# Performance work log

Measured on AMD Instinct MI355X. Metric: run time of the kernel, lower is better.

Reference implementation:

```python
import jax, jax.numpy as jnp
import numpy as np

W_REG = 3.0
N_CAND = 4
IOU_LEN = 15.0
BIG_COST = 1e8


def focal_cost(cls_pred, gt_labels, alpha=0.25, gamma=2.0, eps=1e-12):
    # cls_pred: [B,P,C] logits, gt_labels: [B,T] int -> [B,P,T]
    p = jax.nn.sigmoid(cls_pred)
    neg = -jnp.log(1.0 - p + eps) * (1.0 - alpha) * p ** gamma
    pos = -jnp.log(p + eps) * alpha * (1.0 - p) ** gamma
    B, P, _ = cls_pred.shape
    T = gt_labels.shape[1]
    idx = jnp.broadcast_to(gt_labels[:, None, :], (B, P, T))
    return jnp.take_along_axis(pos, idx, axis=2) - jnp.take_along_axis(neg, idx, axis=2)


def line_iou(pred, target, img_w, length=IOU_LEN):
    # pred: [B,P,O], target: [B,T,O] -> [B,P,T] (unaligned)
    px1, px2 = pred - length, pred + length
    tx1, tx2 = target - length, target + length
    ovr = jnp.minimum(px2[:, :, None, :], tx2[:, None, :, :]) - jnp.maximum(px1[:, :, None, :], tx1[:, None, :, :])
    union = jnp.maximum(px2[:, :, None, :], tx2[:, None, :, :]) - jnp.minimum(px1[:, :, None, :], tx1[:, None, :, :])
    invalid = ((target < 0) | (target >= img_w))[:, None, :, :]
    ovr = jnp.where(invalid, 0.0, ovr)
    union = jnp.where(invalid, 0.0, union)
    return ovr.sum(-1) / (union.sum(-1) + 1e-9)


def clrnet_assign(preds, targets, masks, img_w, img_h):
    B, P, _ = preds.shape
    T = targets.shape[1]
    w = float(img_w - 1)
    h = float(img_h - 1)
    pa = preds.at[..., 3].multiply(w).at[..., 6:].multiply(w)
    ta = targets.at[..., 3].multiply(w).at[..., 6:].multiply(w)
    p_off, t_off = pa[..., 6:], ta[..., 6:]

    # --- distance score (masked mean L1 over valid target x-offsets) ---
    tvalid = (t_off >= 0) & (t_off < img_w)                      # [B,T,O]
    cmask = tvalid[:, None, :, :]                                 # [B,1,T,O]
    clen = jnp.maximum(cmask.sum(-1).astype(pa.dtype), 1.0)      # [B,1,T]
    diff = jnp.abs(p_off[:, :, None, :] - t_off[:, None, :, :]) * cmask  # [B,P,T,O]
    distances = diff.sum(-1) / clen                               # [B,P,T]
    dist_max = jnp.maximum(distances.max(axis=(1, 2), keepdims=True), 1e-8)
    dist_score = 1.0 - distances / dist_max + 0.01

    # --- start-point score (euclidean on (y*(h), x)) ---
    ps = pa[..., 2:4].at[..., 0].multiply(h)
    ts = ta[..., 2:4].at[..., 0].multiply(h)
    start_d = jnp.sqrt(((ps[:, :, None, :] - ts[:, None, :, :]) ** 2).sum(-1))
    start_max = jnp.maximum(start_d.max(axis=(1, 2), keepdims=True), 1e-8)
    start_score = 1.0 - start_d / start_max + 0.01

    # --- theta score ---
    th_d = jnp.abs(pa[..., 4][:, :, None] - ta[..., 4][:, None, :]) * 180.0
    th_max = jnp.maximum(th_d.max(axis=(1, 2), keepdims=True), 1e-8)
    th_score = 1.0 - th_d / th_max + 0.01

    # --- total cost ---
    gt_labels = ta[..., 1].astype(jnp.int32)
    cls_cost = focal_cost(pa[..., :2], gt_labels)
    reg = (jnp.maximum(dist_score, 1e-3) * jnp.maximum(start_score, 1e-3)
           * jnp.maximum(th_score, 1e-3))
    total_cost = -(reg ** 2) * W_REG + cls_cost                   # [B,P,T]
    valid_t = (masks > 0)[:, None, :]                             # [B,1,T]
    total_cost = jnp.where(valid_t, total_cost, BIG_COST)

    # --- dynamic-k from line IoU ---
    liou = jnp.nan_to_num(line_iou(p_off, t_off, img_w), nan=0.0)
    liou = jnp.where(valid_t, liou, 0.0)
    k = min(N_CAND, P)
    topk_ious, _ = jax.lax.top_k(jnp.swapaxes(liou, 1, 2), k)     # [B,T,k]
    dynamic_ks = jnp.maximum(topk_ious.sum(-1).astype(jnp.int32), 1)
    dynamic_ks = jnp.where(masks > 0, dynamic_ks, 0)              # [B,T]

    # --- top-k lowest-cost priors per target, scatter into matching matrix ---
    _, topk_idx = jax.lax.top_k(-jnp.swapaxes(total_cost, 1, 2), k)  # [B,T,k]
    sel = (jnp.arange(k)[None, None, :] < dynamic_ks[:, :, None]).astype(total_cost.dtype)  # [B,T,k]
    one_hot_p = jax.nn.one_hot(topk_idx, P, dtype=total_cost.dtype)  # [B,T,k,P]
    matching = jnp.swapaxes((one_hot_p * sel[..., None]).sum(2), 1, 2)  # [B,P,T]

    # --- conflict resolution: a prior matched to >1 targets keeps argmin-cost one ---
    conflict = matching.sum(-1) > 1                               # [B,P]
    masked_cost = jnp.where(matching == 0, jnp.inf, total_cost)
    best_t = jnp.argmin(masked_cost, axis=2)                      # [B,P]
    new_m = jax.nn.one_hot(best_t, T, dtype=matching.dtype)
    matching = jnp.where(conflict[..., None], new_m, matching)

    has_match = matching.sum(-1) > 0.5
    t_idx = jnp.argmax(matching, axis=2)
    matched = jnp.where(has_match, t_idx, -1).astype(jnp.int32)
    return matched >= 0, matched


def setup_inputs() -> dict:
    key = jax.random.key(0)
    k1, k2, k3 = jax.random.split(key, 3)
    B, P, T, O = 32, 1000, 16, 72
    D = 6 + O
    preds = jax.random.uniform(k1, (B, P, D), dtype=jnp.float32)
    # slightly outside [0,1] so the invalid-offset masking path is exercised
    targets = jax.random.uniform(k2, (B, T, D), dtype=jnp.float32, minval=-0.05, maxval=1.05)
    masks = jax.random.randint(k3, (B, T), 0, 2).astype(jnp.int32)
    return {"preds": preds, "targets": targets, "masks": masks, "img_w": 800, "img_h": 320}


def reference(preds, targets, masks, img_w, img_h):
    return clrnet_assign(preds, targets, masks, img_w, img_h)
```

## Files before the change

### kernel.cpp

```cpp
#include <hip/hip_runtime.h>
#include <math.h>

#define B_ 32
#define P_ 1000
#define T_ 16
#define D_ 78
#define O_ 72
#define NXB 16
#define BIGC 100000000.0f

__global__ __launch_bounds__(1024, 8) void k1(
        const float* __restrict__ preds, const float* __restrict__ targets,
        const int* __restrict__ imgw_p, const int* __restrict__ imgh_p,
        float* __restrict__ dist, float* __restrict__ liou,
        float4* __restrict__ scal4, float* __restrict__ pths,
        float* __restrict__ pmax) {
    __shared__ float pred_s[64 * 81];
    __shared__ float2 tomg[T_ * O_];
    __shared__ float Spart[T_][4][64];
    __shared__ float wmax[16][3];
    __shared__ float cnt_s[T_], clen_s[T_], ts0_s[T_], ts1_s[T_], tth_s[T_];

    const int b = blockIdx.y, bx = blockIdx.x;
    const int p0 = bx * 64;
    const int rows = min(64, P_ - p0);
    const int tid = threadIdx.x;
    const float w = (float)(imgw_p[0] - 1);
    const float h = (float)(imgh_p[0] - 1);
    const float imgwf = (float)imgw_p[0];

    {
        const float4* gbase = (const float4*)(preds + ((size_t)b * P_ + p0) * D_);
        const int n4 = rows * D_ / 4;
        for (int i = tid; i < n4; i += 1024) {
            float4 v = gbase[i];
            int base = i * 4;
            int r = base / D_, c = base - r * D_;
#pragma unroll
            for (int k = 0; k < 4; ++k) {
                int cc = c + k, rr = r;
                if (cc >= D_) { cc -= D_; ++rr; }
                float x = (&v.x)[k];
                if (cc >= 6 || cc == 3) x *= w;
                pred_s[rr * 81 + cc] = x;
            }
        }
    }
    for (int i = tid; i < T_ * O_; i += 1024) {
        int t = i / O_, o = i - t * O_;
        float to = targets[((size_t)b * T_ + t) * D_ + 6 + o] * w;
        float m = (to >= 0.f && to < imgwf) ? 1.f : 0.f;
        tomg[((t >> 2) * O_ + o) * 4 + (t & 3)] = make_float2(to, m);
    }
    __syncthreads();
    if (tid < T_) {
        int t = tid;
        float c = 0.f;
        for (int o = 0; o < O_; ++o) c += tomg[((t >> 2) * O_ + o) * 4 + (t & 3)].y;
        cnt_s[t] = c;
        clen_s[t] = fmaxf(c, 1.f);
        const float* tr = targets + ((size_t)b * T_ + t) * D_;
        ts0_s[t] = tr[2] * h;
        ts1_s[t] = tr[3] * w;
        tth_s[t] = tr[4];
    }
    __syncthreads();

    {
        const int lane = tid & 63;
        const int wv = tid >> 6;
        const int tg = wv & 3;
        const int oq = wv >> 2;
        const float* lrow = pred_s + lane * 81;
        const float4* tg4 = (const float4*)(tomg + (size_t)tg * O_ * 4);
        const int o_lo = oq * 18;
        float S0 = 0.f, S1 = 0.f, S2 = 0.f, S3 = 0.f;
#pragma unroll
        for (int i = 0; i < 18; ++i) {
            int o = o_lo + i;
            float po = lrow[6 + o];
            float4 r0 = tg4[2 * o];
            float4 r1 = tg4[2 * o + 1];
            S0 += r0.y * fabsf(po - r0.x);
            S1 += r0.w * fabsf(po - r0.z);
            S2 += r1.y * fabsf(po - r1.x);
            S3 += r1.w * fabsf(po - r1.z);
        }
        Spart[4 * tg + 0][oq][lane] = S0;
        Spart[4 * tg + 1][oq][lane] = S1;
        Spart[4 * tg + 2][oq][lane] = S2;
        Spart[4 * tg + 3][oq][lane] = S3;
    }
    __syncthreads();

    const int th = tid >> 6, pl = tid & 63;
    const int p = p0 + pl;
    float ldm = 0.f, lsm = 0.f, ltm = 0.f;
    if (pl < rows) {
        float S = ((Spart[th][0][pl] + Spart[th][1][pl]) + Spart[th][2][pl]) + Spart[th][3][pl];
        float dv = S / clen_s[th];
        dist[(size_t)(b * T_ + th) * P_ + p] = dv;
        ldm = dv;
        float c30 = 30.f * cnt_s[th];
        liou[(size_t)(b * T_ + th) * P_ + p] = (c30 - S) / (c30 + S + 1e-9f);
        const float* prow = pred_s + pl * 81;
        float ps0 = prow[2] * h, ps1 = prow[3], pth = prow[4];
        float d0 = ps0 - ts0_s[th], d1 = ps1 - ts1_s[th];
        lsm = sqrtf(d0 * d0 + d1 * d1);
        ltm = fabsf(pth - tth_s[th]) * 180.f;
        if (th == 0) {
            float fc[2];
#pragma unroll
            for (int c = 0; c < 2; ++c) {
                float x = prow[c];
                float pc = 1.f / (1.f + expf(-x));
                float neg = -logf(1.f - pc + 1e-12f) * 0.75f * pc * pc;
                float pos = -logf(pc + 1e-12f) * 0.25f * (1.f - pc) * (1.f - pc);
                fc[c] = pos - neg;
            }
            scal4[(size_t)b * P_ + p] = make_float4(fc[0], fc[1], ps0, ps1);
            pths[(size_t)b * P_ + p] = pth;
        }
    }

    for (int off = 32; off; off >>= 1) {
        ldm = fmaxf(ldm, __shfl_xor(ldm, off, 64));
        lsm = fmaxf(lsm, __shfl_xor(lsm, off, 64));
        ltm = fmaxf(ltm, __shfl_xor(ltm, off, 64));
    }
    if (pl == 0) { wmax[th][0] = ldm; wmax[th][1] = lsm; wmax[th][2] = ltm; }
    __syncthreads();
    if (tid == 0) {
        float m0 = 0.f, m1 = 0.f, m2 = 0.f;
#pragma unroll
        for (int i = 0; i < 16; ++i) {
            m0 = fmaxf(m0, wmax[i][0]);
            m1 = fmaxf(m1, wmax[i][1]);
            m2 = fmaxf(m2, wmax[i][2]);
        }
        float* q = pmax + (size_t)(b * NXB + bx) * 3;
        q[0] = m0; q[1] = m1; q[2] = m2;
    }
}

__global__ __launch_bounds__(256) void k2(
        const float* __restrict__ targets, const int* __restrict__ masks,
        const int* __restrict__ imgw_p, const int* __restrict__ imgh_p,
        const float* __restrict__ dist, const float* __restrict__ liou,
        const float4* __restrict__ scal4, const float* __restrict__ pths,
        const float* __restrict__ pmax,
        int4* __restrict__ sel, float4* __restrict__ selc) {
    __shared__ float costL[1024];
    __shared__ float liouL[1024];

    const int wid = blockIdx.x;
    const int b = wid >> 4, t = wid & 15;
    const int tid = threadIdx.x;

    float dm = 0.f, sm = 0.f, tm = 0.f;
    for (int i = 0; i < NXB; ++i) {
        const float* q = pmax + (size_t)(b * NXB + i) * 3;
        dm = fmaxf(dm, q[0]); sm = fmaxf(sm, q[1]); tm = fmaxf(tm, q[2]);
    }
    dm = fmaxf(dm, 1e-8f); sm = fmaxf(sm, 1e-8f); tm = fmaxf(tm, 1e-8f);

    const float w = (float)(imgw_p[0] - 1);
    const float h = (float)(imgh_p[0] - 1);
    const float* tr = targets + (size_t)(b * T_ + t) * D_;
    const float ts0 = tr[2] * h, ts1 = tr[3] * w, tth = tr[4];
    int lab = (int)tr[1]; lab = lab < 0 ? 0 : (lab > 1 ? 1 : lab);
    const int mk = masks[b * T_ + t];

    const float* drow = dist + (size_t)(b * T_ + t) * P_;
    const float* lrow = liou + (size_t)(b * T_ + t) * P_;
    const float4* s4b = scal4 + (size_t)b * P_;
    const float* ptb = pths + (size_t)b * P_;

#pragma unroll
    for (int i = 0; i < 4; ++i) {
        int p = tid + 256 * i;
        if (p < P_) {
            float d = drow[p];
            float4 s4 = s4b[p];
            float pth = ptb[p];
            float dsc = 1.f - d / dm + 0.01f;
            float d0 = s4.z - ts0, d1 = s4.w - ts1;
            float ssc = 1.f - sqrtf(d0 * d0 + d1 * d1) / sm + 0.01f;
            float tsc = 1.f - fabsf(pth - tth) * 180.f / tm + 0.01f;
            float reg = fmaxf(dsc, 1e-3f) * fmaxf(ssc, 1e-3f) * fmaxf(tsc, 1e-3f);
            float c = -(reg * reg) * 3.f + (lab ? s4.y : s4.x);
            if (mk <= 0) c = BIGC;
            costL[p] = c;
            liouL[p] = lrow[p];
        } else {
            costL[p] = INFINITY;
            liouL[p] = -INFINITY;
        }
    }
    __syncthreads();
    if (tid >= 64) return;

    const int lane = tid;

    float sum = 0.f;
    for (int r = 0; r < 4; ++r) {
        float bv = -INFINITY; int bi = 0x7fffffff;
#pragma unroll
        for (int i = 0; i < 16; ++i) {
            int ix = lane + 64 * i;
            float v = liouL[ix];
            if (v > bv || (v == bv && ix < bi)) { bv = v; bi = ix; }
        }
        for (int off = 32; off; off >>= 1) {
            float ov = __shfl_xor(bv, off, 64);
            int oi = __shfl_xor(bi, off, 64);
            if (ov > bv || (ov == bv && oi < bi)) { bv = ov; bi = oi; }
        }
        sum += bv;
        if ((bi & 63) == lane) liouL[bi] = -INFINITY;
    }
    int dk = 0;
    if (mk > 0) {
        dk = (int)sum;
        if (dk < 1) dk = 1;
        if (dk > 4) dk = 4;
    }

    int s0, s1, s2, s3;
    float c0, c1, c2, c3;
#define ROUNDMIN(sr, cr) {                                                \
        float bv = INFINITY; int bi = 0x7fffffff;                         \
        _Pragma("unroll")                                                 \
        for (int i = 0; i < 16; ++i) {                                    \
            int ix = lane + 64 * i;                                       \
            float v = costL[ix];                                          \
            if (v < bv || (v == bv && ix < bi)) { bv = v; bi = ix; }      \
        }                                                                 \
        for (int off = 32; off; off >>= 1) {                              \
            float ov = __shfl_xor(bv, off, 64);                           \
            int oi = __shfl_xor(bi, off, 64);                             \
            if (ov < bv || (ov == bv && oi < bi)) { bv = ov; bi = oi; }   \
        }                                                                 \
        sr = bi; cr = bv;                                                 \
        if ((bi & 63) == lane) costL[bi] = INFINITY; }
    ROUNDMIN(s0, c0) ROUNDMIN(s1, c1) ROUNDMIN(s2, c2) ROUNDMIN(s3, c3)
#undef ROUNDMIN

    if (lane == 0) {
        sel[wid]  = make_int4(dk > 0 ? s0 : -1, dk > 1 ? s1 : -1,
                              dk > 2 ? s2 : -1, dk > 3 ? s3 : -1);
        selc[wid] = make_float4(c0, c1, c2, c3);
    }
}

__global__ __launch_bounds__(256) void k3(const int* __restrict__ sel,
                                          const float* __restrict__ selc,
                                          int* __restrict__ out) {
    __shared__ int selE[64];
    __shared__ float selC[64];
    const int b = blockIdx.y, cx = blockIdx.x;
    if (threadIdx.x < 64) {
        selE[threadIdx.x] = sel[b * 64 + threadIdx.x];
        selC[threadIdx.x] = selc[b * 64 + threadIdx.x];
    }
    __syncthreads();

    const int p = cx * 250 + threadIdx.x;
    if (threadIdx.x < 250) {
        int matched = -1;
        float best = INFINITY;
#pragma unroll
        for (int t = 0; t < T_; ++t) {
#pragma unroll
            for (int j = 0; j < 4; ++j) {
                if (selE[4 * t + j] == p) {
                    float c = selC[4 * t + j];
                    if (c < best) { best = c; matched = t; }
                }
            }
        }
        out[b * P_ + p] = (matched >= 0) ? 1 : 0;
        out[B_ * P_ + b * P_ + p] = matched;
    }
}

extern "C" void kernel_launch(void* const* d_in, const int* in_sizes, int n_in,
                              void* d_out, int out_size, void* d_ws, size_t ws_size,
                              hipStream_t stream) {
    const float* preds   = (const float*)d_in[0];
    const float* targets = (const float*)d_in[1];
    const int*   masks   = (const int*)d_in[2];
    const int*   imgw    = (const int*)d_in[3];
    const int*   imgh    = (const int*)d_in[4];
    int* out = (int*)d_out;

    char* ws = (char*)d_ws;
    const size_t SZ = (size_t)B_ * T_ * P_ * sizeof(float);
    float*  dist  = (float*)ws;
    float*  liou  = (float*)(ws + SZ);
    float4* scal4 = (float4*)(ws + 2 * SZ);
    float*  pths  = (float*)(ws + 2 * SZ + (size_t)B_ * P_ * 16);
    float*  pmax  = (float*)(ws + 2 * SZ + (size_t)B_ * P_ * 20);
    int4*   sel   = (int4*)(ws + 2 * SZ + (size_t)B_ * P_ * 20 + 8192);
    float4* selc  = (float4*)(ws + 2 * SZ + (size_t)B_ * P_ * 20 + 16384);

    k1<<<dim3(NXB, B_), 1024, 0, stream>>>(preds, targets, imgw, imgh, dist, liou, scal4, pths, pmax);
    k2<<<B_ * T_, 256, 0, stream>>>(targets, masks, imgw, imgh, dist, liou, scal4, pths, pmax, sel, selc);
    k3<<<dim3(4, B_), 256, 0, stream>>>((const int*)sel, (const float*)selc, out);
}
```

Baseline: 34.87 us.

## Store raw L1 sums once and fuse final conflict resolution into k2 via atomic counter

New measurement: 44.76 us. +28.4%, slower.

```diff
diff --git a/kernel.cpp b/kernel.cpp
--- a/kernel.cpp
+++ b/kernel.cpp
@@ -12,9 +12,8 @@
 __global__ __launch_bounds__(1024, 8) void k1(
         const float* __restrict__ preds, const float* __restrict__ targets,
         const int* __restrict__ imgw_p, const int* __restrict__ imgh_p,
-        float* __restrict__ dist, float* __restrict__ liou,
-        float4* __restrict__ scal4, float* __restrict__ pths,
-        float* __restrict__ pmax) {
+        float* __restrict__ Sarr, float4* __restrict__ scal4, float* __restrict__ pths,
+        float* __restrict__ pmax, float* __restrict__ cntg, int* __restrict__ ctr) {
     __shared__ float pred_s[64 * 81];
     __shared__ float2 tomg[T_ * O_];
     __shared__ float Spart[T_][4][64];
@@ -66,6 +65,11 @@
     }
     __syncthreads();
 
+    if (bx == 0) {
+        if (tid < T_) cntg[b * T_ + tid] = cnt_s[tid];
+        if (tid == 32) ctr[b] = 0;
+    }
+
     {
         const int lane = tid & 63;
         const int wv = tid >> 6;
@@ -98,11 +102,9 @@
     float ldm = 0.f, lsm = 0.f, ltm = 0.f;
     if (pl < rows) {
         float S = ((Spart[th][0][pl] + Spart[th][1][pl]) + Spart[th][2][pl]) + Spart[th][3][pl];
+        Sarr[(size_t)(b * T_ + th) * P_ + p] = S;
         float dv = S / clen_s[th];
-        dist[(size_t)(b * T_ + th) * P_ + p] = dv;
         ldm = dv;
-        float c30 = 30.f * cnt_s[th];
-        liou[(size_t)(b * T_ + th) * P_ + p] = (c30 - S) / (c30 + S + 1e-9f);
         const float* prow = pred_s + pl * 81;
         float ps0 = prow[2] * h, ps1 = prow[3], pth = prow[4];
         float d0 = ps0 - ts0_s[th], d1 = ps1 - ts1_s[th];
@@ -146,12 +148,17 @@
 __global__ __launch_bounds__(256) void k2(
         const float* __restrict__ targets, const int* __restrict__ masks,
         const int* __restrict__ imgw_p, const int* __restrict__ imgh_p,
-        const float* __restrict__ dist, const float* __restrict__ liou,
+        const float* __restrict__ Sarr,
         const float4* __restrict__ scal4, const float* __restrict__ pths,
-        const float* __restrict__ pmax,
-        int4* __restrict__ sel, float4* __restrict__ selc) {
+        const float* __restrict__ pmax, const float* __restrict__ cntg,
+        int* __restrict__ ctr,
+        int4* __restrict__ selG, float4* __restrict__ selcG,
+        int* __restrict__ out) {
     __shared__ float costL[1024];
-    __shared__ float liouL[1024];
+    __shared__ float SL[1024];
+    __shared__ int selEL[64];
+    __shared__ float selCL[64];
+    __shared__ int flagS;
 
     const int wid = blockIdx.x;
     const int b = wid >> 4, t = wid & 15;
@@ -170,9 +177,11 @@
     const float ts0 = tr[2] * h, ts1 = tr[3] * w, tth = tr[4];
     int lab = (int)tr[1]; lab = lab < 0 ? 0 : (lab > 1 ? 1 : lab);
     const int mk = masks[b * T_ + t];
-
-    const float* drow = dist + (size_t)(b * T_ + t) * P_;
-    const float* lrow = liou + (size_t)(b * T_ + t) * P_;
+    const float cntv = cntg[b * T_ + t];
+    const float clen = fmaxf(cntv, 1.f);
+    const float c30 = 30.f * cntv;
+
+    const float* Srow = Sarr + (size_t)(b * T_ + t) * P_;
     const float4* s4b = scal4 + (size_t)b * P_;
     const float* ptb = pths + (size_t)b * P_;
 
@@ -180,10 +189,11 @@
     for (int i = 0; i < 4; ++i) {
         int p = tid + 256 * i;
         if (p < P_) {
-            float d = drow[p];
+            float S = Srow[p];
             float4 s4 = s4b[p];
             float pth = ptb[p];
-            float dsc = 1.f - d / dm + 0.01f;
+            float dv = S / clen;
+            float dsc = 1.f - dv / dm + 0.01f;
             float d0 = s4.z - ts0, d1 = s4.w - ts1;
             float ssc = 1.f - sqrtf(d0 * d0 + d1 * d1) / sm + 0.01f;
             float tsc = 1.f - fabsf(pth - tth) * 180.f / tm + 0.01f;
@@ -191,96 +201,96 @@
             float c = -(reg * reg) * 3.f + (lab ? s4.y : s4.x);
             if (mk <= 0) c = BIGC;
             costL[p] = c;
-            liouL[p] = lrow[p];
+            SL[p] = S;
         } else {
             costL[p] = INFINITY;
-            liouL[p] = -INFINITY;
-        }
-    }
-    __syncthreads();
-    if (tid >= 64) return;
-
-    const int lane = tid;
-
-    float sum = 0.f;
-    for (int r = 0; r < 4; ++r) {
-        float bv = -INFINITY; int bi = 0x7fffffff;
-#pragma unroll
-        for (int i = 0; i < 16; ++i) {
-            int ix = lane + 64 * i;
-            float v = liouL[ix];
-            if (v > bv || (v == bv && ix < bi)) { bv = v; bi = ix; }
-        }
-        for (int off = 32; off; off >>= 1) {
-            float ov = __shfl_xor(bv, off, 64);
-            int oi = __shfl_xor(bi, off, 64);
-            if (ov > bv || (ov == bv && oi < bi)) { bv = ov; bi = oi; }
-        }
-        sum += bv;
-        if ((bi & 63) == lane) liouL[bi] = -INFINITY;
-    }
-    int dk = 0;
-    if (mk > 0) {
-        dk = (int)sum;
-        if (dk < 1) dk = 1;
-        if (dk > 4) dk = 4;
-    }
-
-    int s0, s1, s2, s3;
-    float c0, c1, c2, c3;
-#define ROUNDMIN(sr, cr) {                                                \
-        float bv = INFINITY; int bi = 0x7fffffff;                         \
+            SL[p] = INFINITY;
+        }
+    }
+    __syncthreads();
+
+    if (tid < 64) {
+        const int lane = tid;
+
+        float v0, v1, v2, v3;
+#define SROUND(vr) { float bv = INFINITY; int bi = 0x7fffffff;            \
         _Pragma("unroll")                                                 \
-        for (int i = 0; i < 16; ++i) {                                    \
-            int ix = lane + 64 * i;                                       \
-            float v = costL[ix];                                          \
-            if (v < bv || (v == bv && ix < bi)) { bv = v; bi = ix; }      \
-        }                                                                 \
+        for (int i = 0; i < 16; ++i) { int ix = lane + 64 * i;            \
+            float v = SL[ix];                                             \
+            if (v < bv || (v == bv && ix < bi)) { bv = v; bi = ix; } }    \
         for (int off = 32; off; off >>= 1) {                              \
             float ov = __shfl_xor(bv, off, 64);                           \
             int oi = __shfl_xor(bi, off, 64);                             \
             if (ov < bv || (ov == bv && oi < bi)) { bv = ov; bi = oi; }   \
         }                                                                 \
-        sr = bi; cr = bv;                                                 \
-        if ((bi & 63) == lane) costL[bi] = INFINITY; }
-    ROUNDMIN(s0, c0) ROUNDMIN(s1, c1) ROUNDMIN(s2, c2) ROUNDMIN(s3, c3)
-#undef ROUNDMIN
-
-    if (lane == 0) {
-        sel[wid]  = make_int4(dk > 0 ? s0 : -1, dk > 1 ? s1 : -1,
-                              dk > 2 ? s2 : -1, dk > 3 ? s3 : -1);
-        selc[wid] = make_float4(c0, c1, c2, c3);
-    }
-}
-
-__global__ __launch_bounds__(256) void k3(const int* __restrict__ sel,
-                                          const float* __restrict__ selc,
-                                          int* __restrict__ out) {
-    __shared__ int selE[64];
-    __shared__ float selC[64];
-    const int b = blockIdx.y, cx = blockIdx.x;
-    if (threadIdx.x < 64) {
-        selE[threadIdx.x] = sel[b * 64 + threadIdx.x];
-        selC[threadIdx.x] = selc[b * 64 + threadIdx.x];
-    }
-    __syncthreads();
-
-    const int p = cx * 250 + threadIdx.x;
-    if (threadIdx.x < 250) {
-        int matched = -1;
-        float best = INFINITY;
-#pragma unroll
-        for (int t = 0; t < T_; ++t) {
-#pragma unroll
-            for (int j = 0; j < 4; ++j) {
-                if (selE[4 * t + j] == p) {
-                    float c = selC[4 * t + j];
-                    if (c < best) { best = c; matched = t; }
+        vr = bv; if ((bi & 63) == lane) SL[bi] = INFINITY; }
+        SROUND(v0) SROUND(v1) SROUND(v2) SROUND(v3)
+#undef SROUND
+        float l0 = (c30 - v0) / (c30 + v0 + 1e-9f);
+        float l1 = (c30 - v1) / (c30 + v1 + 1e-9f);
+        float l2 = (c30 - v2) / (c30 + v2 + 1e-9f);
+        float l3 = (c30 - v3) / (c30 + v3 + 1e-9f);
+        float sum = ((l0 + l1) + l2) + l3;
+        int dk = 0;
+        if (mk > 0) {
+            dk = (int)sum;
+            if (dk < 1) dk = 1;
+            if (dk > 4) dk = 4;
+        }
+
+        int s0, s1, s2, s3;
+        float c0, c1, c2, c3;
+#define CROUND(sr, cr) { float bv = INFINITY; int bi = 0x7fffffff;        \
+        _Pragma("unroll")                                                 \
+        for (int i = 0; i < 16; ++i) { int ix = lane + 64 * i;            \
+            float v = costL[ix];                                          \
+            if (v < bv || (v == bv && ix < bi)) { bv = v; bi = ix; } }    \
+        for (int off = 32; off; off >>= 1) {                              \
+            float ov = __shfl_xor(bv, off, 64);                           \
+            int oi = __shfl_xor(bi, off, 64);                             \
+            if (ov < bv || (ov == bv && oi < bi)) { bv = ov; bi = oi; }   \
+        }                                                                 \
+        sr = bi; cr = bv; if ((bi & 63) == lane) costL[bi] = INFINITY; }
+        CROUND(s0, c0) CROUND(s1, c1) CROUND(s2, c2) CROUND(s3, c3)
+#undef CROUND
+
+        if (lane == 0) {
+            selG[wid]  = make_int4(dk > 0 ? s0 : -1, dk > 1 ? s1 : -1,
+                                   dk > 2 ? s2 : -1, dk > 3 ? s3 : -1);
+            selcG[wid] = make_float4(c0, c1, c2, c3);
+            int old = __hip_atomic_fetch_add(&ctr[b], 1, __ATOMIC_ACQ_REL,
+                                             __HIP_MEMORY_SCOPE_AGENT);
+            flagS = (old == T_ - 1) ? 1 : 0;
+        }
+    }
+    __syncthreads();
+
+    if (flagS) {
+        if (tid < 64) {
+            selEL[tid] = ((const int*)selG)[b * 64 + tid];
+            selCL[tid] = ((const float*)selcG)[b * 64 + tid];
+        }
+        __syncthreads();
+#pragma unroll
+        for (int i = 0; i < 4; ++i) {
+            int p = tid + 256 * i;
+            if (p < P_) {
+                int matched = -1;
+                float best = INFINITY;
+#pragma unroll
+                for (int t2 = 0; t2 < T_; ++t2) {
+#pragma unroll
+                    for (int j = 0; j < 4; ++j) {
+                        if (selEL[4 * t2 + j] == p) {
+                            float c = selCL[4 * t2 + j];
+                            if (c < best) { best = c; matched = t2; }
+                        }
+                    }
                 }
+                out[b * P_ + p] = (matched >= 0) ? 1 : 0;
+                out[B_ * P_ + b * P_ + p] = matched;
             }
         }
-        out[b * P_ + p] = (matched >= 0) ? 1 : 0;
-        out[B_ * P_ + b * P_ + p] = matched;
     }
 }
 
@@ -295,16 +305,17 @@
     int* out = (int*)d_out;
 
     char* ws = (char*)d_ws;
-    const size_t SZ = (size_t)B_ * T_ * P_ * sizeof(float);
-    float*  dist  = (float*)ws;
-    float*  liou  = (float*)(ws + SZ);
-    float4* scal4 = (float4*)(ws + 2 * SZ);
-    float*  pths  = (float*)(ws + 2 * SZ + (size_t)B_ * P_ * 16);
-    float*  pmax  = (float*)(ws + 2 * SZ + (size_t)B_ * P_ * 20);
-    int4*   sel   = (int4*)(ws + 2 * SZ + (size_t)B_ * P_ * 20 + 8192);
-    float4* selc  = (float4*)(ws + 2 * SZ + (size_t)B_ * P_ * 20 + 16384);
-
-    k1<<<dim3(NXB, B_), 1024, 0, stream>>>(preds, targets, imgw, imgh, dist, liou, scal4, pths, pmax);
-    k2<<<B_ * T_, 256, 0, stream>>>(targets, masks, imgw, imgh, dist, liou, scal4, pths, pmax, sel, selc);
-    k3<<<dim3(4, B_), 256, 0, stream>>>((const int*)sel, (const float*)selc, out);
+    float*  Sarr  = (float*)ws;
+    float4* scal4 = (float4*)(ws + 2048000);
+    float*  pths  = (float*)(ws + 2560000);
+    float*  pmax  = (float*)(ws + 2688000);
+    float*  cntg  = (float*)(ws + 2694144);
+    int*    ctr   = (int*)(ws + 2696192);
+    int4*   selG  = (int4*)(ws + 2696320);
+    float4* selcG = (float4*)(ws + 2704512);
+
+    k1<<<dim3(NXB, B_), 1024, 0, stream>>>(preds, targets, imgw, imgh,
+                                           Sarr, scal4, pths, pmax, cntg, ctr);
+    k2<<<B_ * T_, 256, 0, stream>>>(targets, masks, imgw, imgh, Sarr, scal4, pths,
+                                    pmax, cntg, ctr, selG, selcG, out);
 }
```
